# Optimization experiments

Hardware: AMD Instinct MI355X
Metric: run time of the kernel (lower is better)

The kernel has to match this reference:

```python
import jax, jax.numpy as jnp
import numpy as np


def setup_inputs() -> dict:
    key = jax.random.key(0)
    k1, k2 = jax.random.split(key)
    B, S, K, N = 8, 2048, 2048, 2048
    a = jax.random.normal(k1, (B, S, K), dtype=jnp.float32)
    b = jax.random.normal(k2, (B, K, N), dtype=jnp.float32)
    return {"a": a, "b": b}


def reference(a, b):
    # Per-sample dense: out[i] = a[i] @ b[i], fused as one batched GEMM.
    # a: [B, S, K], b: [B, K, N] -> out: [B, S, N]
    return jnp.einsum('bsk,bkn->bsn', a, b)
```

## Files before the change

### kernel.cpp

```cpp
#include <hip/hip_runtime.h>

#define BATCH 8
#define SDIM 2048
#define KDIM 2048
#define NDIM 2048

typedef __bf16 bf16_t;
typedef bf16_t bf16x4 __attribute__((ext_vector_type(4)));
typedef bf16_t bf16x8 __attribute__((ext_vector_type(8)));
typedef float f32x4 __attribute__((ext_vector_type(4)));
typedef float f32x8 __attribute__((ext_vector_type(8)));
typedef unsigned short u16x8 __attribute__((ext_vector_type(8)));

__device__ __forceinline__ void gl_lds16(const void* g, void* l) {
    __builtin_amdgcn_global_load_lds(
        (__attribute__((address_space(1))) void*)g,
        (__attribute__((address_space(3))) void*)l,
        16, 0, 0);
}

__global__ __launch_bounds__(256)
void cvtA_kernel(const float* __restrict__ A, bf16_t* __restrict__ Abf) {
    const size_t total8 = (size_t)BATCH * SDIM * KDIM / 8;
    const size_t stride = (size_t)gridDim.x * 256;
    for (size_t i = (size_t)blockIdx.x * 256 + threadIdx.x; i < total8; i += stride) {
        f32x8 v = *reinterpret_cast<const f32x8*>(A + i * 8);
        *reinterpret_cast<bf16x8*>(Abf + i * 8) = __builtin_convertvector(v, bf16x8);
    }
}

__global__ __launch_bounds__(256)
void cvtBT_kernel(const float* __restrict__ B, bf16_t* __restrict__ Bt) {
    __shared__ alignas(16) bf16_t T[64][72];
    const int gid = blockIdx.x;
    const int batch = gid & 7;
    const int tile = gid >> 3;
    const int k0g = (tile >> 5) * 64;
    const int n0g = (tile & 31) * 64;
    const float* Bb = B + (size_t)batch * KDIM * NDIM + (size_t)k0g * NDIM + n0g;
    bf16_t* Tb = Bt + (size_t)batch * NDIM * KDIM + (size_t)n0g * KDIM + k0g;

    const int t = threadIdx.x;
    const int kq = t & 15;
    const int nq = t >> 4;
    f32x4 v[4];
#pragma unroll
    for (int r = 0; r < 4; ++r)
        v[r] = *reinterpret_cast<const f32x4*>(Bb + (size_t)(kq * 4 + r) * NDIM + nq * 4);
#pragma unroll
    for (int j = 0; j < 4; ++j) {
        bf16x4 w = {(bf16_t)v[0][j], (bf16_t)v[1][j], (bf16_t)v[2][j], (bf16_t)v[3][j]};
        *reinterpret_cast<bf16x4*>(&T[nq * 4 + j][kq * 4]) = w;
    }
    __syncthreads();
    const int n = t >> 2, kc = t & 3;
    bf16x8 o0 = *reinterpret_cast<const bf16x8*>(&T[n][kc * 16]);
    bf16x8 o1 = *reinterpret_cast<const bf16x8*>(&T[n][kc * 16 + 8]);
    *reinterpret_cast<bf16x8*>(Tb + (size_t)n * KDIM + kc * 16) = o0;
    *reinterpret_cast<bf16x8*>(Tb + (size_t)n * KDIM + kc * 16 + 8) = o1;
}

#define VM4 asm volatile("s_waitcnt vmcnt(4)" ::: "memory")
#define VM0 asm volatile("s_waitcnt vmcnt(0)" ::: "memory")
#define NOOP ((void)0)

__global__ __launch_bounds__(512, 2)
void bgemm_8ph(const bf16_t* __restrict__ A, const bf16_t* __restrict__ Bt,
               float* __restrict__ O) {
    __shared__ alignas(16) bf16_t lds[65536];

    const int tid = threadIdx.x;
    const int gid = blockIdx.x;
    const int batch = gid & 7;
    const int t = gid >> 3;
    const int bm = (t >> 3) * 256;
    const int bn = (t & 7) * 256;

    const int lane = tid & 63;
    const int wid = tid >> 6;
    const int wr = wid >> 2;
    const int wc = wid & 3;
    const int lr = lane & 15;
    const int lq = lane >> 4;

    const bf16_t* Ab = A + (size_t)batch * SDIM * KDIM;
    const bf16_t* Bb = Bt + (size_t)batch * NDIM * KDIM;
    float* Ob = O + (size_t)batch * SDIM * NDIM;

    const bf16_t* aSrc0 = Ab + (size_t)(bm + wid * 32 + lr) * KDIM + lq * 8;
    const bf16_t* aSrc1 = aSrc0 + (size_t)16 * KDIM;
    const bf16_t* bSrc0 = Bb + (size_t)(bn + wid * 32 + lr) * KDIM + lq * 8;
    const bf16_t* bSrc1 = bSrc0 + (size_t)16 * KDIM;

    const int aDst0 = (wid * 2) * 512;
    const int aDst1 = (wid * 2 + 1) * 512;
    const int rdA = lq * 128 + lr * 8;
    const int rdB = 8192 + lq * 128 + lr * 8;

#define STAGE_A(BUF_, KT_) do { \
    gl_lds16(aSrc0 + (size_t)(KT_) * 32, &lds[(BUF_) * 16384 + aDst0]); \
    gl_lds16(aSrc1 + (size_t)(KT_) * 32, &lds[(BUF_) * 16384 + aDst1]); \
} while (0)
#define STAGE_B(BUF_, KT_) do { \
    gl_lds16(bSrc0 + (size_t)(KT_) * 32, &lds[(BUF_) * 16384 + 8192 + aDst0]); \
    gl_lds16(bSrc1 + (size_t)(KT_) * 32, &lds[(BUF_) * 16384 + 8192 + aDst1]); \
} while (0)

    f32x4 acc[8][4];
#pragma unroll
    for (int m = 0; m < 8; ++m)
#pragma unroll
        for (int n = 0; n < 4; ++n)
            acc[m][n] = (f32x4){0.f, 0.f, 0.f, 0.f};

    bf16x8 bfrag[4];

#define PHASE(BUF_, MH_, STAGE_STMT, WAIT_STMT) do { \
    bf16x8 af_[4]; \
    _Pragma("unroll") \
    for (int m_ = 0; m_ < 4; ++m_) \
        af_[m_] = *reinterpret_cast<const bf16x8*>( \
            &lds[(BUF_) * 16384 + (wr * 8 + (MH_) * 4 + m_) * 512 + rdA]); \
    if ((MH_) == 0) { \
        _Pragma("unroll") \
        for (int n_ = 0; n_ < 4; ++n_) \
            bfrag[n_] = *reinterpret_cast<const bf16x8*>( \
                &lds[(BUF_) * 16384 + (wc * 4 + n_) * 512 + rdB]); \
    } \
    STAGE_STMT; \
    __builtin_amdgcn_s_barrier(); \
    __builtin_amdgcn_s_setprio(1); \
    _Pragma("unroll") \
    for (int m_ = 0; m_ < 4; ++m_) \
        _Pragma("unroll") \
        for (int n_ = 0; n_ < 4; ++n_) \
            acc[(MH_) * 4 + m_][n_] = __builtin_amdgcn_mfma_f32_16x16x32_bf16( \
                af_[m_], bfrag[n_], acc[(MH_) * 4 + m_][n_], 0, 0, 0); \
    __builtin_amdgcn_s_setprio(0); \
    WAIT_STMT; \
    __builtin_amdgcn_s_barrier(); \
} while (0)

    STAGE_A(0, 0); STAGE_B(0, 0);
    STAGE_A(1, 1); STAGE_B(1, 1);
    STAGE_A(2, 2); STAGE_B(2, 2);
    VM4;
    __builtin_amdgcn_s_barrier();

#pragma unroll 1
    for (int it = 0; it < 15; ++it) {
        const int k4 = it * 4;
        PHASE(0, 0, STAGE_A(3, k4 + 3), NOOP);
        PHASE(0, 1, STAGE_B(3, k4 + 3), NOOP);
        PHASE(1, 0, STAGE_A(0, k4 + 4), NOOP);
        PHASE(1, 1, STAGE_B(0, k4 + 4), VM4);
        PHASE(2, 0, STAGE_A(1, k4 + 5), NOOP);
        PHASE(2, 1, STAGE_B(1, k4 + 5), NOOP);
        PHASE(3, 0, STAGE_A(2, k4 + 6), NOOP);
        PHASE(3, 1, STAGE_B(2, k4 + 6), VM4);
    }
    PHASE(0, 0, STAGE_A(3, 63), NOOP);
    PHASE(0, 1, STAGE_B(3, 63), NOOP);
    PHASE(1, 0, NOOP, NOOP);
    PHASE(1, 1, NOOP, VM0);
    PHASE(2, 0, NOOP, NOOP);
    PHASE(2, 1, NOOP, NOOP);
    PHASE(3, 0, NOOP, NOOP);
    PHASE(3, 1, NOOP, NOOP);

#pragma unroll
    for (int m = 0; m < 8; ++m) {
        const int row0 = bm + wr * 128 + m * 16 + lq * 4;
#pragma unroll
        for (int n = 0; n < 4; ++n) {
            const int col = bn + wc * 64 + n * 16 + lr;
#pragma unroll
            for (int j = 0; j < 4; ++j)
                Ob[(size_t)(row0 + j) * NDIM + col] = acc[m][n][j];
        }
    }
#undef PHASE
#undef STAGE_A
#undef STAGE_B
}

__device__ __forceinline__ unsigned short f2bf(float f) {
    unsigned int u = __builtin_bit_cast(unsigned int, f);
    u += 0x7fffu + ((u >> 16) & 1u);
    return (unsigned short)(u >> 16);
}

__global__ __launch_bounds__(256, 2)
void bgemm_fused(const float* __restrict__ A, const float* __restrict__ B,
                 float* __restrict__ O) {
    __shared__ alignas(16) unsigned short Asl[2][4 * 128 * 8];
    __shared__ alignas(16) unsigned short Bsl[2][4 * 128 * 8];
    const int tid = threadIdx.x;
    const int gid = blockIdx.x;
    const int batch = gid & 7;
    const int t = gid >> 3;
    const int bm = (t >> 4) * 128;
    const int bn = (t & 15) * 128;
    const float* Ab = A + (size_t)batch * SDIM * KDIM;
    const float* Bb = B + (size_t)batch * KDIM * NDIM;
    float* Ob = O + (size_t)batch * SDIM * NDIM;
    const int lane = tid & 63;
    const int wid = tid >> 6;
    const int wr = wid >> 1, wc = wid & 1;
    const int lr = lane & 15, lq = lane >> 4;
    const int r0 = tid & 127, h0 = tid >> 7;
    u16x8 areg[2], breg[2];
    f32x4 acc[4][4];
#pragma unroll
    for (int m = 0; m < 4; ++m)
#pragma unroll
        for (int n = 0; n < 4; ++n) acc[m][n] = (f32x4){0.f, 0.f, 0.f, 0.f};
    auto stage_regs = [&](int kt) {
        const int k0 = kt * 32;
        const float* ap = Ab + (size_t)(bm + r0) * KDIM + k0 + h0 * 16;
        float4 a0 = *reinterpret_cast<const float4*>(ap + 0);
        float4 a1 = *reinterpret_cast<const float4*>(ap + 4);
        float4 a2 = *reinterpret_cast<const float4*>(ap + 8);
        float4 a3 = *reinterpret_cast<const float4*>(ap + 12);
        u16x8 u;
        u[0]=f2bf(a0.x);u[1]=f2bf(a0.y);u[2]=f2bf(a0.z);u[3]=f2bf(a0.w);
        u[4]=f2bf(a1.x);u[5]=f2bf(a1.y);u[6]=f2bf(a1.z);u[7]=f2bf(a1.w);
        areg[0]=u;
        u[0]=f2bf(a2.x);u[1]=f2bf(a2.y);u[2]=f2bf(a2.z);u[3]=f2bf(a2.w);
        u[4]=f2bf(a3.x);u[5]=f2bf(a3.y);u[6]=f2bf(a3.z);u[7]=f2bf(a3.w);
        areg[1]=u;
        const float* bp = Bb + (size_t)(k0 + h0 * 16) * NDIM + bn + r0;
        float f[16];
#pragma unroll
        for (int j = 0; j < 16; ++j) f[j] = bp[(size_t)j * NDIM];
        u16x8 v;
#pragma unroll
        for (int j = 0; j < 8; ++j) v[j] = f2bf(f[j]);
        breg[0] = v;
#pragma unroll
        for (int j = 0; j < 8; ++j) v[j] = f2bf(f[8 + j]);
        breg[1] = v;
    };
    auto regs_to_lds = [&](int b) {
#pragma unroll
        for (int o = 0; o < 2; ++o) {
            *reinterpret_cast<u16x8*>(&Asl[b][((h0*2+o)*128 + r0)*8]) = areg[o];
            *reinterpret_cast<u16x8*>(&Bsl[b][((h0*2+o)*128 + r0)*8]) = breg[o];
        }
    };
    stage_regs(0);
    regs_to_lds(0);
    int buf = 0;
    for (int kt = 0; kt < KDIM / 32; ++kt) {
        if (kt + 1 < KDIM / 32) stage_regs(kt + 1);
        __syncthreads();
        bf16x8 af[4], bfv[4];
#pragma unroll
        for (int m = 0; m < 4; ++m)
            af[m] = *reinterpret_cast<const bf16x8*>(&Asl[buf][(lq*128 + wr*64 + m*16 + lr)*8]);
#pragma unroll
        for (int n = 0; n < 4; ++n)
            bfv[n] = *reinterpret_cast<const bf16x8*>(&Bsl[buf][(lq*128 + wc*64 + n*16 + lr)*8]);
#pragma unroll
        for (int m = 0; m < 4; ++m)
#pragma unroll
            for (int n = 0; n < 4; ++n)
                acc[m][n] = __builtin_amdgcn_mfma_f32_16x16x32_bf16(af[m], bfv[n], acc[m][n], 0, 0, 0);
        if (kt + 1 < KDIM / 32) regs_to_lds(buf ^ 1);
        buf ^= 1;
    }
#pragma unroll
    for (int m = 0; m < 4; ++m) {
        const int row0 = bm + wr * 64 + m * 16 + lq * 4;
#pragma unroll
        for (int n = 0; n < 4; ++n) {
            const int col = bn + wc * 64 + n * 16 + lr;
#pragma unroll
            for (int j = 0; j < 4; ++j)
                Ob[(size_t)(row0 + j) * NDIM + col] = acc[m][n][j];
        }
    }
}

extern "C" void kernel_launch(void* const* d_in, const int* in_sizes, int n_in,
                              void* d_out, int out_size, void* d_ws, size_t ws_size,
                              hipStream_t stream) {
    const float* a = (const float*)d_in[0];
    const float* b = (const float*)d_in[1];
    float* o = (float*)d_out;
    const size_t half = (size_t)BATCH * SDIM * KDIM * sizeof(bf16_t);
    if (ws_size >= 2 * half) {
        bf16_t* Abf = (bf16_t*)d_ws;
        bf16_t* Bt = (bf16_t*)((char*)d_ws + half);
        hipLaunchKernelGGL(cvtA_kernel, dim3(4096), dim3(256), 0, stream, a, Abf);
        hipLaunchKernelGGL(cvtBT_kernel, dim3(8192), dim3(256), 0, stream, b, Bt);
        hipLaunchKernelGGL(bgemm_8ph, dim3(512), dim3(512), 0, stream, Abf, Bt, o);
    } else {
        hipLaunchKernelGGL(bgemm_fused, dim3(2048), dim3(256), 0, stream, a, b, o);
    }
}
```

Before: 244.5 us.

## Replace 8-phase split pipeline with 4-stage ring, one barrier per k-tile

```diff
diff --git a/kernel.cpp b/kernel.cpp
--- a/kernel.cpp
+++ b/kernel.cpp
@@ -60,13 +60,14 @@
     *reinterpret_cast<bf16x8*>(Tb + (size_t)n * KDIM + kc * 16 + 8) = o1;
 }
 
+#define VM8 asm volatile("s_waitcnt vmcnt(8)" ::: "memory")
 #define VM4 asm volatile("s_waitcnt vmcnt(4)" ::: "memory")
 #define VM0 asm volatile("s_waitcnt vmcnt(0)" ::: "memory")
 #define NOOP ((void)0)
 
 __global__ __launch_bounds__(512, 2)
-void bgemm_8ph(const bf16_t* __restrict__ A, const bf16_t* __restrict__ Bt,
-               float* __restrict__ O) {
+void bgemm_ring(const bf16_t* __restrict__ A, const bf16_t* __restrict__ Bt,
+                float* __restrict__ O) {
     __shared__ alignas(16) bf16_t lds[65536];
 
     const int tid = threadIdx.x;
@@ -97,11 +98,9 @@
     const int rdA = lq * 128 + lr * 8;
     const int rdB = 8192 + lq * 128 + lr * 8;
 
-#define STAGE_A(BUF_, KT_) do { \
+#define STAGE(BUF_, KT_) do { \
     gl_lds16(aSrc0 + (size_t)(KT_) * 32, &lds[(BUF_) * 16384 + aDst0]); \
     gl_lds16(aSrc1 + (size_t)(KT_) * 32, &lds[(BUF_) * 16384 + aDst1]); \
-} while (0)
-#define STAGE_B(BUF_, KT_) do { \
     gl_lds16(bSrc0 + (size_t)(KT_) * 32, &lds[(BUF_) * 16384 + 8192 + aDst0]); \
     gl_lds16(bSrc1 + (size_t)(KT_) * 32, &lds[(BUF_) * 16384 + 8192 + aDst1]); \
 } while (0)
@@ -113,60 +112,44 @@
         for (int n = 0; n < 4; ++n)
             acc[m][n] = (f32x4){0.f, 0.f, 0.f, 0.f};
 
-    bf16x8 bfrag[4];
-
-#define PHASE(BUF_, MH_, STAGE_STMT, WAIT_STMT) do { \
-    bf16x8 af_[4]; \
+#define BODY(BUF_, STAGE_STMT, VM_STMT) do { \
+    VM_STMT; \
+    __builtin_amdgcn_s_barrier(); \
+    STAGE_STMT; \
+    bf16x8 af_[8], bf_[4]; \
     _Pragma("unroll") \
-    for (int m_ = 0; m_ < 4; ++m_) \
+    for (int m_ = 0; m_ < 8; ++m_) \
         af_[m_] = *reinterpret_cast<const bf16x8*>( \
-            &lds[(BUF_) * 16384 + (wr * 8 + (MH_) * 4 + m_) * 512 + rdA]); \
-    if ((MH_) == 0) { \
+            &lds[(BUF_) * 16384 + (wr * 8 + m_) * 512 + rdA]); \
+    _Pragma("unroll") \
+    for (int n_ = 0; n_ < 4; ++n_) \
+        bf_[n_] = *reinterpret_cast<const bf16x8*>( \
+            &lds[(BUF_) * 16384 + (wc * 4 + n_) * 512 + rdB]); \
+    __builtin_amdgcn_s_setprio(1); \
+    _Pragma("unroll") \
+    for (int m_ = 0; m_ < 8; ++m_) \
         _Pragma("unroll") \
         for (int n_ = 0; n_ < 4; ++n_) \
-            bfrag[n_] = *reinterpret_cast<const bf16x8*>( \
-                &lds[(BUF_) * 16384 + (wc * 4 + n_) * 512 + rdB]); \
-    } \
-    STAGE_STMT; \
-    __builtin_amdgcn_s_barrier(); \
-    __builtin_amdgcn_s_setprio(1); \
-    _Pragma("unroll") \
-    for (int m_ = 0; m_ < 4; ++m_) \
-        _Pragma("unroll") \
-        for (int n_ = 0; n_ < 4; ++n_) \
-            acc[(MH_) * 4 + m_][n_] = __builtin_amdgcn_mfma_f32_16x16x32_bf16( \
-                af_[m_], bfrag[n_], acc[(MH_) * 4 + m_][n_], 0, 0, 0); \
+            acc[m_][n_] = __builtin_amdgcn_mfma_f32_16x16x32_bf16( \
+                af_[m_], bf_[n_], acc[m_][n_], 0, 0, 0); \
     __builtin_amdgcn_s_setprio(0); \
-    WAIT_STMT; \
-    __builtin_amdgcn_s_barrier(); \
 } while (0)
 
-    STAGE_A(0, 0); STAGE_B(0, 0);
-    STAGE_A(1, 1); STAGE_B(1, 1);
-    STAGE_A(2, 2); STAGE_B(2, 2);
-    VM4;
-    __builtin_amdgcn_s_barrier();
+    STAGE(0, 0);
+    STAGE(1, 1);
+    STAGE(2, 2);
 
 #pragma unroll 1
-    for (int it = 0; it < 15; ++it) {
-        const int k4 = it * 4;
-        PHASE(0, 0, STAGE_A(3, k4 + 3), NOOP);
-        PHASE(0, 1, STAGE_B(3, k4 + 3), NOOP);
-        PHASE(1, 0, STAGE_A(0, k4 + 4), NOOP);
-        PHASE(1, 1, STAGE_B(0, k4 + 4), VM4);
-        PHASE(2, 0, STAGE_A(1, k4 + 5), NOOP);
-        PHASE(2, 1, STAGE_B(1, k4 + 5), NOOP);
-        PHASE(3, 0, STAGE_A(2, k4 + 6), NOOP);
-        PHASE(3, 1, STAGE_B(2, k4 + 6), VM4);
-    }
-    PHASE(0, 0, STAGE_A(3, 63), NOOP);
-    PHASE(0, 1, STAGE_B(3, 63), NOOP);
-    PHASE(1, 0, NOOP, NOOP);
-    PHASE(1, 1, NOOP, VM0);
-    PHASE(2, 0, NOOP, NOOP);
-    PHASE(2, 1, NOOP, NOOP);
-    PHASE(3, 0, NOOP, NOOP);
-    PHASE(3, 1, NOOP, NOOP);
+    for (int j4 = 0; j4 < 60; j4 += 4) {
+        BODY(0, STAGE(3, j4 + 3), VM8);
+        BODY(1, STAGE(0, j4 + 4), VM8);
+        BODY(2, STAGE(1, j4 + 5), VM8);
+        BODY(3, STAGE(2, j4 + 6), VM8);
+    }
+    BODY(0, STAGE(3, 63), VM8);
+    BODY(1, NOOP, VM8);
+    BODY(2, NOOP, VM4);
+    BODY(3, NOOP, VM0);
 
 #pragma unroll
     for (int m = 0; m < 8; ++m) {
@@ -179,9 +162,8 @@
                 Ob[(size_t)(row0 + j) * NDIM + col] = acc[m][n][j];
         }
     }
-#undef PHASE
-#undef STAGE_A
-#undef STAGE_B
+#undef BODY
+#undef STAGE
 }
 
 __device__ __forceinline__ unsigned short f2bf(float f) {
@@ -294,7 +276,7 @@
         bf16_t* Bt = (bf16_t*)((char*)d_ws + half);
         hipLaunchKernelGGL(cvtA_kernel, dim3(4096), dim3(256), 0, stream, a, Abf);
         hipLaunchKernelGGL(cvtBT_kernel, dim3(8192), dim3(256), 0, stream, b, Bt);
-        hipLaunchKernelGGL(bgemm_8ph, dim3(512), dim3(512), 0, stream, Abf, Bt, o);
+        hipLaunchKernelGGL(bgemm_ring, dim3(512), dim3(512), 0, stream, Abf, Bt, o);
     } else {
         hipLaunchKernelGGL(bgemm_fused, dim3(2048), dim3(256), 0, stream, a, b, o);
     }
```

Measured after the change: 254.0 us (median of 3 runs). 1.04x slower.
